# Performance work log

Measured on AMD Instinct MI355X. Metric: run time of the kernel, lower is better.

## Reference

```python
import jax, jax.numpy as jnp
import numpy as np

EPS = 1e-5

# The 8 fixed sobel kernels from the original module. Summing convolutions with
# the same input equals one convolution with the summed kernel, so we embed the
# four 3x3 kernels (pad=1) into 5x5 (pad=2) and precombine everything into a
# single depthwise 5x5 kernel (exactly the math of detect_edge_1/2 summed).
_K3 = [
    [[2, 4, 2], [0, 0, 0], [-2, -4, -2]],
    [[4, 2, 0], [2, 0, -2], [0, -2, -4]],
    [[2, 0, -2], [4, 0, -4], [2, 0, -2]],
    [[0, -2, -4], [2, 0, -2], [4, 2, 0]],
]
_K5 = [
    [[0, 0, 0, 0, 0], [0, -2, -4, -2, 0], [-1, -4, 0, 4, 1], [0, 2, 4, 2, 0], [0, 0, 0, 0, 0]],
    [[0, 0, -1, 0, 0], [0, -2, -4, 2, 0], [0, -4, 0, 4, 0], [0, -2, 4, 2, 0], [0, 0, 1, 0, 0]],
    [[0, 0, 1, 0, 0], [0, -2, 4, 2, 0], [0, -4, 0, 4, 0], [0, -2, -4, 2, 0], [0, 0, -1, 0, 0]],
    [[0, 0, 0, 0, 0], [0, 2, 4, 2, 0], [-1, -4, 0, 4, 1], [0, -2, -4, -2, 0], [0, 0, 0, 0, 0]],
]

def _combined_sobel_kernel():
    k = np.zeros((5, 5), dtype=np.float32)
    for k3 in _K3:
        k[1:4, 1:4] += np.asarray(k3, dtype=np.float32)
    for k5 in _K5:
        k += np.asarray(k5, dtype=np.float32)
    return jnp.asarray(k)

SOBEL_K = _combined_sobel_kernel()  # [5,5]


def _conv2d(x, w, b, pad):
    # x: [N,C,H,W], w: [O,I,kh,kw]
    y = jax.lax.conv_general_dilated(
        x, w, window_strides=(1, 1), padding=[(pad, pad), (pad, pad)],
        dimension_numbers=('NCHW', 'OIHW', 'NCHW'))
    return y + b[None, :, None, None]


def _bn_relu(y, gamma, beta):
    # BatchNorm2d in training mode: per-channel batch stats over (N,H,W),
    # biased variance, eps=1e-5.
    m = jnp.mean(y, axis=(0, 2, 3), keepdims=True)
    v = jnp.mean(jnp.square(y - m), axis=(0, 2, 3), keepdims=True)
    yn = (y - m) * jax.lax.rsqrt(v + EPS)
    return jax.nn.relu(yn * gamma[None, :, None, None] + beta[None, :, None, None])


def _single_conv(x, w, b, gamma, beta, pad):
    return _bn_relu(_conv2d(x, w, b, pad), gamma, beta)


def _sobel(x):
    # Fused depthwise conv replacing the per-channel loops over 8 kernels.
    C = x.shape[1]
    w = jnp.broadcast_to(SOBEL_K[None, None], (C, 1, 5, 5))
    return jax.lax.conv_general_dilated(
        x, w, window_strides=(1, 1), padding=[(2, 2), (2, 2)],
        dimension_numbers=('NCHW', 'OIHW', 'NCHW'), feature_group_count=C)


def setup_inputs() -> dict:
    key = jax.random.key(0)
    ks = jax.random.split(key, 16)
    Cin, Cout = 64, 128
    Ch = Cout // 2
    B, H, W = 8, 160, 160
    s = 0.05
    d = {
        'input_f': jax.random.normal(ks[0], (B, Cin, H, W), jnp.float32),
        'w1': jax.random.normal(ks[1], (Cout, Cin, 1, 1), jnp.float32) * s,
        'b1': jnp.zeros((Cout,), jnp.float32),
        'g1': jnp.ones((Cout,), jnp.float32),
        'be1': jnp.zeros((Cout,), jnp.float32),
        'w2': jax.random.normal(ks[2], (Ch, Cout, 3, 3), jnp.float32) * s,
        'b2': jnp.zeros((Ch,), jnp.float32),
        'g2': jnp.ones((Ch,), jnp.float32),
        'be2': jnp.zeros((Ch,), jnp.float32),
        'w3': jax.random.normal(ks[3], (Ch, Ch, 3, 3), jnp.float32) * s,
        'b3': jnp.zeros((Ch,), jnp.float32),
        'g3': jnp.ones((Ch,), jnp.float32),
        'be3': jnp.zeros((Ch,), jnp.float32),
        'w4': jax.random.normal(ks[4], (Ch, Cin, 3, 3), jnp.float32) * s,
        'b4': jnp.zeros((Ch,), jnp.float32),
        'g4': jnp.ones((Ch,), jnp.float32),
        'be4': jnp.zeros((Ch,), jnp.float32),
    }
    return d


def reference(input_f, w1, b1, g1, be1, w2, b2, g2, be2, w3, b3, g3, be3, w4, b4, g4, be4):
    c1 = _single_conv(input_f, w1, b1, g1, be1, pad=0)   # [B,Cout,H,W]
    c2 = _single_conv(c1, w2, b2, g2, be2, pad=1)        # [B,Cout//2,H,W]
    edge = _sobel(c2)                                    # depthwise sobel sum
    c3 = _single_conv(edge, w3, b3, g3, be3, pad=1)
    skip = _single_conv(input_f, w4, b4, g4, be4, pad=1)
    return jnp.concatenate([skip, c3], axis=1)           # [B,Cout,H,W]
```

## Files before the change

### kernel.cpp

```cpp
#include <hip/hip_runtime.h>

typedef unsigned short u16;
typedef unsigned int u32;
typedef __attribute__((ext_vector_type(8))) short bf16x8;
typedef __attribute__((ext_vector_type(4))) float f32x4;

#define WD 160
#define HW 25600
#define NPIXF 204800.0f
#define BNEPS 1e-5f
#define SLOTB 6553600ll
#define BATB  13107200ll

__device__ __forceinline__ float bf2f(u16 u){ return __uint_as_float(((u32)u)<<16); }
__device__ __forceinline__ u16 f2bf(float f){ u32 x=__float_as_uint(f); return (u16)((x + 0x7FFFu + ((x>>16)&1u))>>16); }
__device__ __forceinline__ u32 pack2(float a,float b){ return (u32)f2bf(a) | ((u32)f2bf(b)<<16); }

__device__ __forceinline__ f32x4 MF(bf16x8 a, bf16x8 b, f32x4 c){
  return __builtin_amdgcn_mfma_f32_16x16x32_bf16(a, b, c, 0, 0, 0);
}
__device__ __forceinline__ void gload16(const void* g, void* l){
  __builtin_amdgcn_global_load_lds((const __attribute__((address_space(1))) void*)(g),
                                   (__attribute__((address_space(3))) void*)(l), 16, 0, 0);
}

__global__ __launch_bounds__(256) void k_prepw(
    const float* __restrict__ w1, const float* __restrict__ w2,
    const float* __restrict__ w3, const float* __restrict__ w4,
    u16* __restrict__ wp1, u16* __restrict__ wp2,
    u16* __restrict__ wp3, u16* __restrict__ wp4)
{
  int t = blockIdx.x*256 + threadIdx.x;
  if (t < 8192){
    int i = t&7, oc = (t>>3)&127, kc = (t>>10)&3, icb = t>>12;
    wp1[t] = f2bf(w1[oc*64 + icb*32 + kc*8 + i]);
  }
  int u = t - 8192;
  if (u >= 0 && u < 73728){
    int i = u&7, oc = (u>>3)&63, kc = (u>>9)&3, v = u>>11;
    int icb = (v*57)>>9; int tap = v - icb*9;
    wp2[u] = f2bf(w2[(oc*128 + icb*32 + kc*8 + i)*9 + tap]);
  }
  int u3 = t - (8192+73728);
  if (u3 >= 0 && u3 < 36864){
    int k = u3&31, oc = (u3>>5)&63, v = u3>>11;
    int icb = (v >= 9) ? 1 : 0; int tap = v - icb*9;
    wp3[u3] = f2bf(w3[(oc*64 + icb*32 + k)*9 + tap]);
    wp4[u3] = f2bf(w4[(oc*64 + icb*32 + k)*9 + tap]);
  }
}

__global__ __launch_bounds__(256,2) void k_conv1(
    const float* __restrict__ x, const u16* __restrict__ wp1,
    char* __restrict__ dout, float* __restrict__ stats, int nslot)
{
  __shared__ __align__(16) char Xs[2][8192];
  const int tid = threadIdx.x, lane = tid&63, w = tid>>6;
  const int l15 = lane&15, kc = lane>>4;
  const int b = blockIdx.y, px0 = blockIdx.x*128;
  const float* xb = x + (size_t)b*64*HW;

#pragma unroll 4
  for (int it=0; it<16; ++it){
    int s = it*256 + tid;
    int icb = s >> 11, sl = s & 2047;
    int icp = sl >> 7, px = sl & 127;
    const float* p = xb + (size_t)(icb*32 + icp*2)*HW + px0 + px;
    float v0 = p[0], v1 = p[HW];
    int phys = px*64 + (((icp>>2) ^ ((px>>1)&3))<<4) + (icp&3)*4;
    *(u32*)(Xs[icb] + phys) = pack2(v0, v1);
  }
  __syncthreads();

  f32x4 acc[4][4];
  for (int t=0;t<4;++t) for (int o=0;o<4;++o) acc[t][o] = (f32x4){0.f,0.f,0.f,0.f};
  const int och = (w>>1)*64;
  int a1off[4];
  for (int t=0;t<4;++t){
    int px = (w&1)*64 + t*16 + l15;
    a1off[t] = px*64 + ((kc ^ ((px>>1)&3))<<4);
  }
#pragma unroll
  for (int icb=0; icb<2; ++icb){
    bf16x8 a[4], bw[4];
#pragma unroll
    for (int t=0;t<4;++t) a[t] = *(const bf16x8*)(Xs[icb] + a1off[t]);
#pragma unroll
    for (int o=0;o<4;++o)
      bw[o] = *(const bf16x8*)(wp1 + ((size_t)(icb*4 + kc)*128 + och + o*16 + l15)*8);
#pragma unroll
    for (int t=0;t<4;++t)
#pragma unroll
      for (int o=0;o<4;++o)
        acc[t][o] = MF(a[t], bw[o], acc[t][o]);
  }

  u16* c1 = (u16*)(dout + (size_t)b*BATB);
  float sa[4]={0,0,0,0}, sq[4]={0,0,0,0};
  for (int t=0;t<4;++t){
    int pxb = px0 + (w&1)*64 + t*16 + kc*4;
    for (int o=0;o<4;++o){
      int oc = och + o*16 + l15;
#pragma unroll
      for (int r=0;r<4;++r){
        float v = acc[t][o][r];
        c1[(size_t)(pxb + r)*128 + oc] = f2bf(v);
        sa[o]+=v; sq[o]+=v*v;
      }
    }
  }
  const int slot = (blockIdx.y*gridDim.x + blockIdx.x) & (nslot-1);
  for (int o=0;o<4;++o){
    float s1_=sa[o], s2_=sq[o];
    s1_+=__shfl_xor(s1_,16); s2_+=__shfl_xor(s2_,16);
    s1_+=__shfl_xor(s1_,32); s2_+=__shfl_xor(s2_,32);
    if (lane < 16){
      float* p = stats + ((size_t)slot*128 + och + o*16 + l15)*4;
      atomicAdd(p, s1_); atomicAdd(p+1, s2_);
    }
  }
}

__global__ void k_fold(const float* __restrict__ src, float* __restrict__ dst, int nslot){
  int c = threadIdx.x; if (c >= 128) return;
  float sm=0.f, sq=0.f;
  for (int s=0;s<nslot;++s){ const float* p = src + ((size_t)s*128 + c)*4; sm+=p[0]; sq+=p[1]; }
  dst[c*2] = sm; dst[c*2+1] = sq;
}

__global__ __launch_bounds__(256) void k_bn1(
    char* __restrict__ dout, const float* __restrict__ f1,
    const float* __restrict__ g1, const float* __restrict__ be1)
{
  __shared__ float asc[128], abi[128];
  int tid = threadIdx.x;
  if (tid < 128){
    float m = f1[tid*2]/NPIXF;
    float v = f1[tid*2+1]/NPIXF - m*m;
    float sc = g1[tid]*rsqrtf(v + BNEPS);
    asc[tid] = sc; abi[tid] = be1[tid] - m*sc;
  }
  __syncthreads();
  int b = blockIdx.y;
  size_t r = ((size_t)blockIdx.x*256 + tid)*8;
  int c0 = (int)(r & 127);
  const u16* src = (const u16*)(dout + (size_t)b*BATB) + r;
  u16* dst = (u16*)(dout + (size_t)b*BATB + SLOTB) + r;
  uint4 q = *(const uint4*)src;
  u32 wv[4] = {q.x,q.y,q.z,q.w};
#pragma unroll
  for (int j=0;j<4;++j){
    float lo = bf2f((u16)(wv[j]&0xFFFFu)), hi = bf2f((u16)(wv[j]>>16));
    lo = fmaxf(0.f, lo*asc[c0+2*j]   + abi[c0+2*j]);
    hi = fmaxf(0.f, hi*asc[c0+2*j+1] + abi[c0+2*j+1]);
    wv[j] = pack2(lo, hi);
  }
  *(uint4*)dst = make_uint4(wv[0],wv[1],wv[2],wv[3]);
}

__global__ __launch_bounds__(256,2) void k_conv2(
    char* __restrict__ dout, const u16* __restrict__ wp2,
    float* __restrict__ statsO, const u16* __restrict__ zeros, int nslot)
{
  __shared__ __align__(16) char Xs[24576];
  const int tid = threadIdx.x, lane = tid&63, w = tid>>6;
  const int l15 = lane&15, kc = lane>>4;
  const int b = blockIdx.z, gx0 = blockIdx.x*32, gy0 = blockIdx.y*8;
  const u16* c1a = (const u16*)(dout + (size_t)b*BATB + SLOTB);
  u16* raw2 = (u16*)(dout + (size_t)b*BATB);

  f32x4 acc[4][4];
  for (int t=0;t<4;++t) for (int o=0;o<4;++o) acc[t][o] = (f32x4){0.f,0.f,0.f,0.f};

  int xon[2][3];
  for (int h=0;h<2;++h) for (int dx=0;dx<3;++dx){
    int xi = l15 + h*16 + dx;
    xon[h][dx] = xi*64 + ((kc ^ ((xi>>1)&3))<<4);
  }

  for (int icb=0; icb<4; ++icb){
    __syncthreads();
    for (int it=0; it<6; ++it){
      int s = it*256 + tid;
      int p = s>>2, sub = s&3;
      int yy = (int)(((u32)p*241u)>>13);
      int xi = p - yy*34;
      int gy = gy0 - 1 + yy, gx = gx0 - 1 + xi;
      int c = sub ^ ((xi>>1)&3);
      const u16* src = zeros + ((tid&63)<<3);
      if (p < 340 && (unsigned)gy < 160u && (unsigned)gx < 160u)
        src = c1a + ((size_t)(gy*WD+gx)*128 + icb*32 + c*8);
      gload16(src, Xs + (it*256 + (tid & ~63))*16);
    }
    asm volatile("s_waitcnt vmcnt(0)" ::: "memory");
    __syncthreads();
#pragma unroll
    for (int tap=0; tap<9; ++tap){
      const int dy = tap/3, dx = tap - dy*3;
      bf16x8 a[4], bw[4];
#pragma unroll
      for (int o=0;o<4;++o)
        bw[o] = *(const bf16x8*)(wp2 + ((size_t)((icb*9 + tap)*4 + kc)*64 + o*16 + l15)*8);
#pragma unroll
      for (int t=0;t<4;++t)
        a[t] = *(const bf16x8*)(Xs + (2*w + (t>>1) + dy)*2176 + xon[t&1][dx]);
#pragma unroll
      for (int t=0;t<4;++t)
#pragma unroll
        for (int o=0;o<4;++o)
          acc[t][o] = MF(a[t], bw[o], acc[t][o]);
    }
  }

  float sa[4]={0,0,0,0}, sq[4]={0,0,0,0};
  for (int t=0;t<4;++t){
    int gy = gy0 + 2*w + (t>>1);
    int gxb = gx0 + (t&1)*16 + kc*4;
    for (int o=0;o<4;++o){
      int oc = o*16 + l15;
#pragma unroll
      for (int r=0;r<4;++r){
        float v = acc[t][o][r];
        raw2[(size_t)(gy*WD + gxb + r)*64 + oc] = f2bf(v);
        sa[o]+=v; sq[o]+=v*v;
      }
    }
  }
  int slot = (blockIdx.x + 5*(blockIdx.y + 20*blockIdx.z)) & (nslot-1);
  for (int o=0;o<4;++o){
    float s1_=sa[o], s2_=sq[o];
    s1_+=__shfl_xor(s1_,16); s2_+=__shfl_xor(s2_,16);
    s1_+=__shfl_xor(s1_,32); s2_+=__shfl_xor(s2_,32);
    if (lane<16){
      float* p = statsO + ((size_t)slot*128 + o*16 + l15)*4;
      atomicAdd(p,s1_); atomicAdd(p+1,s2_);
    }
  }
}

__global__ __launch_bounds__(256) void k_sobel(
    char* __restrict__ dout, const float* __restrict__ f2,
    const float* __restrict__ g2, const float* __restrict__ be2)
{
  __shared__ float asc[64], abi[64];
  int tid = threadIdx.x;
  if (tid < 64){
    float m = f2[tid*2]/NPIXF, v = f2[tid*2+1]/NPIXF - m*m;
    float sc = g2[tid]*rsqrtf(v+BNEPS);
    asc[tid]=sc; abi[tid]=be2[tid]-m*sc;
  }
  __syncthreads();
  int b = blockIdx.z, cb = blockIdx.y;
  int px = blockIdx.x*256 + tid;
  int y = (int)(((u32)px*52429u)>>23);
  int x = px - y*WD;
  const u16* raw2 = (const u16*)(dout + (size_t)b*BATB);
  u16* edge = (u16*)(dout + (size_t)b*BATB + 3276800);
  float av[8] = {0,0,0,0,0,0,0,0};
  auto TAP = [&](int dy, int dx, float wt){
    int yy = y+dy, xx = x+dx;
    if ((unsigned)yy>=160u || (unsigned)xx>=160u) return;
    uint4 q = *(const uint4*)(raw2 + ((size_t)(yy*WD+xx)*64 + cb*8));
    u32 ww[4] = {q.x,q.y,q.z,q.w};
#pragma unroll
    for (int j=0;j<4;++j){
      float lo = bf2f((u16)(ww[j]&0xFFFFu)), hi = bf2f((u16)(ww[j]>>16));
      lo = fmaxf(0.f, lo*asc[cb*8+2*j]   + abi[cb*8+2*j]);
      hi = fmaxf(0.f, hi*asc[cb*8+2*j+1] + abi[cb*8+2*j+1]);
      av[2*j]   += wt*lo;
      av[2*j+1] += wt*hi;
    }
  };
  TAP(-1,-1,4.f); TAP(-1,0,4.f);
  TAP(0,-2,-2.f); TAP(0,-1,-8.f); TAP(0,1,8.f); TAP(0,2,2.f);
  TAP(1,0,-4.f);  TAP(1,1,-4.f);
  uint4 o;
  o.x = pack2(av[0],av[1]); o.y = pack2(av[2],av[3]);
  o.z = pack2(av[4],av[5]); o.w = pack2(av[6],av[7]);
  *(uint4*)(edge + ((size_t)px*64 + cb*8)) = o;
}

__global__ __launch_bounds__(256,2) void k_conv34(
    char* __restrict__ dout, const float* __restrict__ x,
    const u16* __restrict__ wp3, const u16* __restrict__ wp4,
    float* __restrict__ st3, float* __restrict__ st4,
    const u16* __restrict__ zeros, int nslot)
{
  __shared__ __align__(16) char Xs[49152];
  const int tid = threadIdx.x, lane = tid&63, w = tid>>6;
  const int l15 = lane&15, kc = lane>>4;
  const int bz = blockIdx.z, b = bz>>1, job = bz&1;
  const int gx0 = blockIdx.x*32, gy0 = blockIdx.y*8;
  const u16* wp = job ? wp4 : wp3;
  float* statsO = job ? st4 : st3;
  float* out = job ? (float*)(dout + (size_t)b*BATB)
                   : (float*)(dout + (size_t)b*BATB + SLOTB);

  if (job){
    const float* xb = x + (size_t)b*64*HW;
#pragma unroll 4
    for (int it=0; it<43; ++it){
      int s = it*256 + tid; if (s >= 10880) break;
      int icb = (s >= 5440) ? 1 : 0;
      int sl = s - icb*5440;
      int yq = (int)(((u32)(sl>>5)*965u)>>14);
      int rem = sl - yq*544;
      int icp = (int)(((u32)rem*241u)>>13);
      int xi = rem - icp*34;
      int gy = gy0-1+yq, gx = gx0-1+xi;
      float v0=0.f, v1=0.f;
      if ((unsigned)gy<160u && (unsigned)gx<160u){
        const float* p = xb + (size_t)(icb*32 + icp*2)*HW + gy*WD + gx;
        v0 = p[0]; v1 = p[HW];
      }
      int phys = icb*24576 + (yq*34 + xi)*64 + (((icp>>2) ^ ((xi>>1)&3))<<4) + (icp&3)*4;
      *(u32*)(Xs + phys) = pack2(v0, v1);
    }
  } else {
    const u16* edge = (const u16*)(dout + (size_t)b*BATB + 3276800);
    for (int it=0; it<12; ++it){
      int s = it*256 + tid;
      int icb = s >> 11;
      icb = (s >= 1536) ? 1 : 0;
      int sl = s - icb*1536;
      int p = sl>>2, sub = sl&3;
      int yy = (int)(((u32)p*241u)>>13);
      int xi = p - yy*34;
      int gy = gy0-1+yy, gx = gx0-1+xi;
      int c = sub ^ ((xi>>1)&3);
      const u16* src = zeros + ((tid&63)<<3);
      if (p<340 && (unsigned)gy<160u && (unsigned)gx<160u)
        src = edge + ((size_t)(gy*WD+gx)*64 + icb*32 + c*8);
      gload16(src, Xs + (it*256 + (tid & ~63))*16);
    }
    asm volatile("s_waitcnt vmcnt(0)" ::: "memory");
  }
  __syncthreads();

  f32x4 acc[4][4];
  for (int m=0;m<4;++m) for (int t=0;t<4;++t) acc[m][t] = (f32x4){0.f,0.f,0.f,0.f};
  int xon[2][3];
  for (int h=0;h<2;++h) for (int dx=0;dx<3;++dx){
    int xi = l15 + h*16 + dx;
    xon[h][dx] = xi*64 + ((kc ^ ((xi>>1)&3))<<4);
  }

#pragma unroll
  for (int icb=0; icb<2; ++icb){
#pragma unroll
    for (int tap=0; tap<9; ++tap){
      const int dy = tap/3, dx = tap - dy*3;
      bf16x8 a[4], bv[4];
#pragma unroll
      for (int m=0;m<4;++m)
        a[m] = *(const bf16x8*)(wp + ((size_t)((icb*9+tap)*64 + m*16 + l15)*32 + kc*8));
#pragma unroll
      for (int t=0;t<4;++t)
        bv[t] = *(const bf16x8*)(Xs + icb*24576 + (2*w + (t>>1) + dy)*2176 + xon[t&1][dx]);
#pragma unroll
      for (int m=0;m<4;++m)
#pragma unroll
        for (int t=0;t<4;++t)
          acc[m][t] = MF(a[m], bv[t], acc[m][t]);
    }
  }

  float sa[4][4], sq[4][4];
  for (int m=0;m<4;++m) for (int r=0;r<4;++r){ sa[m][r]=0.f; sq[m][r]=0.f; }
  for (int m=0;m<4;++m){
    for (int t=0;t<4;++t){
      int gy = gy0 + 2*w + (t>>1);
      int gx = gx0 + (t&1)*16 + l15;
#pragma unroll
      for (int r=0;r<4;++r){
        float v = acc[m][t][r];
        out[(size_t)(m*16 + kc*4 + r)*HW + gy*WD + gx] = v;
        sa[m][r]+=v; sq[m][r]+=v*v;
      }
    }
  }
  int slot = (blockIdx.x + 5*(blockIdx.y + 20*blockIdx.z)) & (nslot-1);
  for (int m=0;m<4;++m)
    for (int r=0;r<4;++r){
      float s1_=sa[m][r], s2_=sq[m][r];
      s1_+=__shfl_xor(s1_,1); s2_+=__shfl_xor(s2_,1);
      s1_+=__shfl_xor(s1_,2); s2_+=__shfl_xor(s2_,2);
      s1_+=__shfl_xor(s1_,4); s2_+=__shfl_xor(s2_,4);
      s1_+=__shfl_xor(s1_,8); s2_+=__shfl_xor(s2_,8);
      if (l15==0){
        float* p = statsO + ((size_t)slot*128 + m*16 + kc*4 + r)*4;
        atomicAdd(p,s1_); atomicAdd(p+1,s2_);
      }
    }
}

__global__ __launch_bounds__(256) void k_bnrelu(
    float* __restrict__ io, const float* __restrict__ f3, const float* __restrict__ f4,
    const float* __restrict__ g3, const float* __restrict__ be3,
    const float* __restrict__ g4, const float* __restrict__ be4)
{
  size_t e = ((size_t)blockIdx.x*256 + threadIdx.x)*8;
  int cg = (int)((e/HW) & 127);
  float* p = io + (size_t)blockIdx.y*3276800 + e;
  float sm,sq,gg,bb;
  if (cg>=64){ int c=cg-64; sm=f3[c*2]; sq=f3[c*2+1]; gg=g3[c]; bb=be3[c]; }
  else       {             sm=f4[cg*2]; sq=f4[cg*2+1]; gg=g4[cg]; bb=be4[cg]; }
  float m = sm/NPIXF;
  float v = sq/NPIXF - m*m;
  float sc = gg*rsqrtf(v + BNEPS);
  float bi = bb - m*sc;
  float4 a = *(float4*)p;
  float4 bq = *(float4*)(p+4);
  a.x=fmaxf(0.f,a.x*sc+bi); a.y=fmaxf(0.f,a.y*sc+bi);
  a.z=fmaxf(0.f,a.z*sc+bi); a.w=fmaxf(0.f,a.w*sc+bi);
  bq.x=fmaxf(0.f,bq.x*sc+bi); bq.y=fmaxf(0.f,bq.y*sc+bi);
  bq.z=fmaxf(0.f,bq.z*sc+bi); bq.w=fmaxf(0.f,bq.w*sc+bi);
  *(float4*)p = a;
  *(float4*)(p+4) = bq;
}

extern "C" void kernel_launch(void* const* d_in, const int* in_sizes, int n_in,
                              void* d_out, int out_size, void* d_ws, size_t ws_size,
                              hipStream_t stream)
{
  const float* x   = (const float*)d_in[0];
  const float* w1  = (const float*)d_in[1];
  const float* g1  = (const float*)d_in[3];
  const float* be1 = (const float*)d_in[4];
  const float* w2  = (const float*)d_in[5];
  const float* g2  = (const float*)d_in[7];
  const float* be2 = (const float*)d_in[8];
  const float* w3  = (const float*)d_in[9];
  const float* g3  = (const float*)d_in[11];
  const float* be3 = (const float*)d_in[12];
  const float* w4  = (const float*)d_in[13];
  const float* g4  = (const float*)d_in[15];
  const float* be4 = (const float*)d_in[16];
  (void)in_sizes; (void)n_in; (void)out_size;

  int nslot = 32;
  auto need = [&](int ns)->size_t{
    return (size_t)4*ns*128*4*4 + 4096 + (size_t)(8192+73728+36864+36864)*2 + 1024;
  };
  while (nslot > 1 && need(nslot) > ws_size) nslot >>= 1;
  if (need(nslot) > ws_size) return;

  char* ws = (char*)d_ws;
  float* S = (float*)ws;
  size_t stg = (size_t)nslot*128*4;
  float* S0=S, *S1=S+stg, *S2=S+2*stg, *S3=S+3*stg;
  float* F = S + 4*stg;
  u16* wp1 = (u16*)(F + 1024);
  u16* wp2 = wp1 + 8192;
  u16* wp3 = wp2 + 73728;
  u16* wp4 = wp3 + 36864;
  u16* zeros = wp4 + 36864;

  hipMemsetAsync(S, 0, 4*stg*sizeof(float), stream);
  hipMemsetAsync(zeros, 0, 1024, stream);

  k_prepw<<<464, 256, 0, stream>>>(w1, w2, w3, w4, wp1, wp2, wp3, wp4);
  k_conv1<<<dim3(200,8), 256, 0, stream>>>(x, wp1, (char*)d_out, S0, nslot);
  k_fold<<<1, 128, 0, stream>>>(S0, F, nslot);
  k_bn1<<<dim3(1600,8), 256, 0, stream>>>((char*)d_out, F, g1, be1);
  k_conv2<<<dim3(5,20,8), 256, 0, stream>>>((char*)d_out, wp2, S1, zeros, nslot);
  k_fold<<<1, 128, 0, stream>>>(S1, F+256, nslot);
  k_sobel<<<dim3(100,8,8), 256, 0, stream>>>((char*)d_out, F+256, g2, be2);
  k_conv34<<<dim3(5,20,16), 256, 0, stream>>>((char*)d_out, x, wp3, wp4, S2, S3, zeros, nslot);
  k_fold<<<1, 128, 0, stream>>>(S2, F+512, nslot);
  k_fold<<<1, 128, 0, stream>>>(S3, F+768, nslot);
  k_bnrelu<<<dim3(1600,8), 256, 0, stream>>>((float*)d_out, F+512, F+768, g3, be3, g4, be4);
}
```

Baseline: 392.4 us.

## Fuse BN1 into conv2 staging, fold stats in sobel, vectorize input loads

Removes the separate BN1+ReLU pass by applying the scale/bias while conv2 stages its input tile into LDS, which drops one full read/write sweep of the conv1 activations. The separate fold kernel after conv2 goes away because the sobel kernel reduces the per-slot statistics itself, and the two final fold launches are merged into one. Conv1 and the skip branch of conv34 now load x with float4 vectors, and conv34 stages one channel block at a time to halve its LDS footprint. When the workspace is large enough, the edge tensor is placed there; otherwise conv34 is split into two launches. The cost is register-staged loads in conv2 in place of direct-to-LDS loads, plus extra synchronisation.

```diff
diff --git a/kernel.cpp b/kernel.cpp
--- a/kernel.cpp
+++ b/kernel.cpp
@@ -54,21 +54,28 @@
     const float* __restrict__ x, const u16* __restrict__ wp1,
     char* __restrict__ dout, float* __restrict__ stats, int nslot)
 {
-  __shared__ __align__(16) char Xs[2][8192];
+  __shared__ __align__(16) char Xs[16384];
   const int tid = threadIdx.x, lane = tid&63, w = tid>>6;
   const int l15 = lane&15, kc = lane>>4;
   const int b = blockIdx.y, px0 = blockIdx.x*128;
   const float* xb = x + (size_t)b*64*HW;
 
-#pragma unroll 4
-  for (int it=0; it<16; ++it){
-    int s = it*256 + tid;
-    int icb = s >> 11, sl = s & 2047;
-    int icp = sl >> 7, px = sl & 127;
-    const float* p = xb + (size_t)(icb*32 + icp*2)*HW + px0 + px;
-    float v0 = p[0], v1 = p[HW];
-    int phys = px*64 + (((icp>>2) ^ ((px>>1)&3))<<4) + (icp&3)*4;
-    *(u32*)(Xs[icb] + phys) = pack2(v0, v1);
+#pragma unroll
+  for (int q=0; q<4; ++q){
+    int s = q*256 + tid;
+    int icb = s >> 9, sl = s & 511;
+    int cp = sl >> 5, px4 = sl & 31;
+    const float* pa = xb + (size_t)(icb*32 + cp*2)*HW + px0 + px4*4;
+    float4 va = *(const float4*)pa;
+    float4 vb = *(const float4*)(pa + HW);
+    float fa[4] = {va.x, va.y, va.z, va.w};
+    float fb[4] = {vb.x, vb.y, vb.z, vb.w};
+#pragma unroll
+    for (int e=0;e<4;++e){
+      int px = px4*4+e;
+      int phys = icb*8192 + px*64 + (((cp>>2) ^ ((px>>1)&3))<<4) + (cp&3)*4;
+      *(u32*)(Xs + phys) = pack2(fa[e], fb[e]);
+    }
   }
   __syncthreads();
 
@@ -84,7 +91,7 @@
   for (int icb=0; icb<2; ++icb){
     bf16x8 a[4], bw[4];
 #pragma unroll
-    for (int t=0;t<4;++t) a[t] = *(const bf16x8*)(Xs[icb] + a1off[t]);
+    for (int t=0;t<4;++t) a[t] = *(const bf16x8*)(Xs + icb*8192 + a1off[t]);
 #pragma unroll
     for (int o=0;o<4;++o)
       bw[o] = *(const bf16x8*)(wp1 + ((size_t)(icb*4 + kc)*128 + och + o*16 + l15)*8);
@@ -128,46 +135,36 @@
   dst[c*2] = sm; dst[c*2+1] = sq;
 }
 
-__global__ __launch_bounds__(256) void k_bn1(
-    char* __restrict__ dout, const float* __restrict__ f1,
-    const float* __restrict__ g1, const float* __restrict__ be1)
-{
-  __shared__ float asc[128], abi[128];
-  int tid = threadIdx.x;
-  if (tid < 128){
-    float m = f1[tid*2]/NPIXF;
-    float v = f1[tid*2+1]/NPIXF - m*m;
-    float sc = g1[tid]*rsqrtf(v + BNEPS);
-    asc[tid] = sc; abi[tid] = be1[tid] - m*sc;
-  }
-  __syncthreads();
-  int b = blockIdx.y;
-  size_t r = ((size_t)blockIdx.x*256 + tid)*8;
-  int c0 = (int)(r & 127);
-  const u16* src = (const u16*)(dout + (size_t)b*BATB) + r;
-  u16* dst = (u16*)(dout + (size_t)b*BATB + SLOTB) + r;
-  uint4 q = *(const uint4*)src;
-  u32 wv[4] = {q.x,q.y,q.z,q.w};
-#pragma unroll
-  for (int j=0;j<4;++j){
-    float lo = bf2f((u16)(wv[j]&0xFFFFu)), hi = bf2f((u16)(wv[j]>>16));
-    lo = fmaxf(0.f, lo*asc[c0+2*j]   + abi[c0+2*j]);
-    hi = fmaxf(0.f, hi*asc[c0+2*j+1] + abi[c0+2*j+1]);
-    wv[j] = pack2(lo, hi);
-  }
-  *(uint4*)dst = make_uint4(wv[0],wv[1],wv[2],wv[3]);
+__global__ void k_fold23(const float* __restrict__ s2, const float* __restrict__ s3,
+                         float* __restrict__ f23, int nslot){
+  int t = threadIdx.x;
+  const float* src = (t < 128) ? s2 : s3;
+  int c = t & 127;
+  float sm=0.f, sq=0.f;
+  for (int s=0;s<nslot;++s){ const float* p = src + ((size_t)s*128 + c)*4; sm+=p[0]; sq+=p[1]; }
+  f23[t*2] = sm; f23[t*2+1] = sq;
 }
 
 __global__ __launch_bounds__(256,2) void k_conv2(
     char* __restrict__ dout, const u16* __restrict__ wp2,
-    float* __restrict__ statsO, const u16* __restrict__ zeros, int nslot)
-{
-  __shared__ __align__(16) char Xs[24576];
+    const float* __restrict__ f0, const float* __restrict__ g1,
+    const float* __restrict__ be1,
+    float* __restrict__ statsO, int nslot)
+{
+  __shared__ __align__(16) char Xs[21760];
+  __shared__ __align__(16) float scbi[128][2];
   const int tid = threadIdx.x, lane = tid&63, w = tid>>6;
   const int l15 = lane&15, kc = lane>>4;
   const int b = blockIdx.z, gx0 = blockIdx.x*32, gy0 = blockIdx.y*8;
-  const u16* c1a = (const u16*)(dout + (size_t)b*BATB + SLOTB);
-  u16* raw2 = (u16*)(dout + (size_t)b*BATB);
+  const u16* c1raw = (const u16*)(dout + (size_t)b*BATB);
+  u16* raw2 = (u16*)(dout + (size_t)b*BATB + SLOTB);
+
+  if (tid < 128){
+    float m = f0[tid*2]/NPIXF;
+    float v = f0[tid*2+1]/NPIXF - m*m;
+    float sc = g1[tid]*rsqrtf(v + BNEPS);
+    scbi[tid][0] = sc; scbi[tid][1] = be1[tid] - m*sc;
+  }
 
   f32x4 acc[4][4];
   for (int t=0;t<4;++t) for (int o=0;o<4;++o) acc[t][o] = (f32x4){0.f,0.f,0.f,0.f};
@@ -178,21 +175,32 @@
     xon[h][dx] = xi*64 + ((kc ^ ((xi>>1)&3))<<4);
   }
 
+  __syncthreads();
   for (int icb=0; icb<4; ++icb){
-    __syncthreads();
-    for (int it=0; it<6; ++it){
-      int s = it*256 + tid;
+    if (icb) __syncthreads();
+    for (int s = tid; s < 1360; s += 256){
       int p = s>>2, sub = s&3;
       int yy = (int)(((u32)p*241u)>>13);
       int xi = p - yy*34;
       int gy = gy0 - 1 + yy, gx = gx0 - 1 + xi;
       int c = sub ^ ((xi>>1)&3);
-      const u16* src = zeros + ((tid&63)<<3);
-      if (p < 340 && (unsigned)gy < 160u && (unsigned)gx < 160u)
-        src = c1a + ((size_t)(gy*WD+gx)*128 + icb*32 + c*8);
-      gload16(src, Xs + (it*256 + (tid & ~63))*16);
-    }
-    asm volatile("s_waitcnt vmcnt(0)" ::: "memory");
+      uint4 o4 = make_uint4(0,0,0,0);
+      if ((unsigned)gy < 160u && (unsigned)gx < 160u){
+        int cb = icb*32 + c*8;
+        uint4 q = *(const uint4*)(c1raw + ((size_t)(gy*WD+gx)*128 + cb));
+        u32 ww[4] = {q.x,q.y,q.z,q.w};
+        u32 ro[4];
+#pragma unroll
+        for (int j=0;j<4;++j){
+          float lo = bf2f((u16)(ww[j]&0xFFFFu)), hi = bf2f((u16)(ww[j]>>16));
+          lo = fmaxf(0.f, lo*scbi[cb+2*j][0]   + scbi[cb+2*j][1]);
+          hi = fmaxf(0.f, hi*scbi[cb+2*j+1][0] + scbi[cb+2*j+1][1]);
+          ro[j] = pack2(lo, hi);
+        }
+        o4 = make_uint4(ro[0],ro[1],ro[2],ro[3]);
+      }
+      *(uint4*)(Xs + p*64 + sub*16) = o4;
+    }
     __syncthreads();
 #pragma unroll
     for (int tap=0; tap<9; ++tap){
@@ -239,23 +247,35 @@
 }
 
 __global__ __launch_bounds__(256) void k_sobel(
-    char* __restrict__ dout, const float* __restrict__ f2,
-    const float* __restrict__ g2, const float* __restrict__ be2)
-{
-  __shared__ float asc[64], abi[64];
+    char* __restrict__ dout, const float* __restrict__ S1,
+    const float* __restrict__ g2, const float* __restrict__ be2,
+    u16* __restrict__ edge_base, long ebstride, int nslot)
+{
+  __shared__ float ascS[8], abiS[8];
   int tid = threadIdx.x;
+  int b = blockIdx.z, cb = blockIdx.y;
   if (tid < 64){
-    float m = f2[tid*2]/NPIXF, v = f2[tid*2+1]/NPIXF - m*m;
-    float sc = g2[tid]*rsqrtf(v+BNEPS);
-    asc[tid]=sc; abi[tid]=be2[tid]-m*sc;
+    int c = cb*8 + (tid&7);
+    float sm=0.f, sq=0.f;
+    for (int s = tid>>3; s < nslot; s += 8){
+      const float* p = S1 + ((size_t)s*128 + c)*4;
+      sm += p[0]; sq += p[1];
+    }
+    sm += __shfl_xor(sm, 8);  sq += __shfl_xor(sq, 8);
+    sm += __shfl_xor(sm, 16); sq += __shfl_xor(sq, 16);
+    sm += __shfl_xor(sm, 32); sq += __shfl_xor(sq, 32);
+    if (tid < 8){
+      float m = sm/NPIXF, v = sq/NPIXF - m*m;
+      float sc = g2[c]*rsqrtf(v+BNEPS);
+      ascS[tid] = sc; abiS[tid] = be2[c] - m*sc;
+    }
   }
   __syncthreads();
-  int b = blockIdx.z, cb = blockIdx.y;
   int px = blockIdx.x*256 + tid;
   int y = (int)(((u32)px*52429u)>>23);
   int x = px - y*WD;
-  const u16* raw2 = (const u16*)(dout + (size_t)b*BATB);
-  u16* edge = (u16*)(dout + (size_t)b*BATB + 3276800);
+  const u16* raw2 = (const u16*)(dout + (size_t)b*BATB + SLOTB);
+  u16* edge = edge_base + (size_t)b*ebstride;
   float av[8] = {0,0,0,0,0,0,0,0};
   auto TAP = [&](int dy, int dx, float wt){
     int yy = y+dy, xx = x+dx;
@@ -265,8 +285,8 @@
 #pragma unroll
     for (int j=0;j<4;++j){
       float lo = bf2f((u16)(ww[j]&0xFFFFu)), hi = bf2f((u16)(ww[j]>>16));
-      lo = fmaxf(0.f, lo*asc[cb*8+2*j]   + abi[cb*8+2*j]);
-      hi = fmaxf(0.f, hi*asc[cb*8+2*j+1] + abi[cb*8+2*j+1]);
+      lo = fmaxf(0.f, lo*ascS[2*j]   + abiS[2*j]);
+      hi = fmaxf(0.f, hi*ascS[2*j+1] + abiS[2*j+1]);
       av[2*j]   += wt*lo;
       av[2*j+1] += wt*hi;
     }
@@ -284,58 +304,22 @@
     char* __restrict__ dout, const float* __restrict__ x,
     const u16* __restrict__ wp3, const u16* __restrict__ wp4,
     float* __restrict__ st3, float* __restrict__ st4,
-    const u16* __restrict__ zeros, int nslot)
-{
-  __shared__ __align__(16) char Xs[49152];
+    const u16* __restrict__ zeros, const u16* __restrict__ edge_base,
+    long ebstride, int nslot, int mode)
+{
+  __shared__ __align__(16) char Xs[24576];
   const int tid = threadIdx.x, lane = tid&63, w = tid>>6;
   const int l15 = lane&15, kc = lane>>4;
-  const int bz = blockIdx.z, b = bz>>1, job = bz&1;
+  int b, job;
+  if (mode == 2){ b = blockIdx.z>>1; job = blockIdx.z&1; }
+  else          { b = blockIdx.z;    job = mode; }
   const int gx0 = blockIdx.x*32, gy0 = blockIdx.y*8;
   const u16* wp = job ? wp4 : wp3;
   float* statsO = job ? st4 : st3;
   float* out = job ? (float*)(dout + (size_t)b*BATB)
                    : (float*)(dout + (size_t)b*BATB + SLOTB);
-
-  if (job){
-    const float* xb = x + (size_t)b*64*HW;
-#pragma unroll 4
-    for (int it=0; it<43; ++it){
-      int s = it*256 + tid; if (s >= 10880) break;
-      int icb = (s >= 5440) ? 1 : 0;
-      int sl = s - icb*5440;
-      int yq = (int)(((u32)(sl>>5)*965u)>>14);
-      int rem = sl - yq*544;
-      int icp = (int)(((u32)rem*241u)>>13);
-      int xi = rem - icp*34;
-      int gy = gy0-1+yq, gx = gx0-1+xi;
-      float v0=0.f, v1=0.f;
-      if ((unsigned)gy<160u && (unsigned)gx<160u){
-        const float* p = xb + (size_t)(icb*32 + icp*2)*HW + gy*WD + gx;
-        v0 = p[0]; v1 = p[HW];
-      }
-      int phys = icb*24576 + (yq*34 + xi)*64 + (((icp>>2) ^ ((xi>>1)&3))<<4) + (icp&3)*4;
-      *(u32*)(Xs + phys) = pack2(v0, v1);
-    }
-  } else {
-    const u16* edge = (const u16*)(dout + (size_t)b*BATB + 3276800);
-    for (int it=0; it<12; ++it){
-      int s = it*256 + tid;
-      int icb = s >> 11;
-      icb = (s >= 1536) ? 1 : 0;
-      int sl = s - icb*1536;
-      int p = sl>>2, sub = sl&3;
-      int yy = (int)(((u32)p*241u)>>13);
-      int xi = p - yy*34;
-      int gy = gy0-1+yy, gx = gx0-1+xi;
-      int c = sub ^ ((xi>>1)&3);
-      const u16* src = zeros + ((tid&63)<<3);
-      if (p<340 && (unsigned)gy<160u && (unsigned)gx<160u)
-        src = edge + ((size_t)(gy*WD+gx)*64 + icb*32 + c*8);
-      gload16(src, Xs + (it*256 + (tid & ~63))*16);
-    }
-    asm volatile("s_waitcnt vmcnt(0)" ::: "memory");
-  }
-  __syncthreads();
+  const float* xb = x + (size_t)b*64*HW;
+  const u16* edge = edge_base + (size_t)b*ebstride;
 
   f32x4 acc[4][4];
   for (int m=0;m<4;++m) for (int t=0;t<4;++t) acc[m][t] = (f32x4){0.f,0.f,0.f,0.f};
@@ -345,8 +329,58 @@
     xon[h][dx] = xi*64 + ((kc ^ ((xi>>1)&3))<<4);
   }
 
-#pragma unroll
   for (int icb=0; icb<2; ++icb){
+    if (icb) __syncthreads();
+    if (job){
+      for (int s = tid; s < 1600; s += 256){
+        int s10 = (int)(((u32)s*6554u)>>16);
+        int q = s - s10*10;
+        int cp = (int)(((u32)s10*6554u)>>16);
+        int yq = s10 - cp*10;
+        int gy = gy0 - 1 + yq;
+        int gxq = gx0 - 4 + q*4;
+        float fa[4] = {0,0,0,0}, fb[4] = {0,0,0,0};
+        if ((unsigned)gy < 160u){
+          const float* pa = xb + (size_t)(icb*32 + cp*2)*HW + gy*WD + gxq;
+          if (gxq >= 0 && gxq + 3 < 160){
+            float4 va = *(const float4*)pa;
+            float4 vb = *(const float4*)(pa + HW);
+            fa[0]=va.x; fa[1]=va.y; fa[2]=va.z; fa[3]=va.w;
+            fb[0]=vb.x; fb[1]=vb.y; fb[2]=vb.z; fb[3]=vb.w;
+          } else {
+#pragma unroll
+            for (int e=0;e<4;++e){
+              int gx = gxq + e;
+              if ((unsigned)gx < 160u){ fa[e] = pa[e]; fb[e] = pa[e + HW]; }
+            }
+          }
+        }
+#pragma unroll
+        for (int e=0;e<4;++e){
+          int xi = gxq + e - (gx0 - 1);
+          if ((unsigned)xi < 34u){
+            int phys = (yq*34 + xi)*64 + (((cp>>2) ^ ((xi>>1)&3))<<4) + (cp&3)*4;
+            *(u32*)(Xs + phys) = pack2(fa[e], fb[e]);
+          }
+        }
+      }
+    } else {
+      for (int it=0; it<6; ++it){
+        int s = it*256 + tid;
+        int p = s>>2, sub = s&3;
+        int yy = (int)(((u32)p*241u)>>13);
+        int xi = p - yy*34;
+        int gy = gy0-1+yy, gx = gx0-1+xi;
+        int c = sub ^ ((xi>>1)&3);
+        const u16* src = zeros + ((tid&63)<<3);
+        if (p<340 && (unsigned)gy<160u && (unsigned)gx<160u)
+          src = edge + ((size_t)(gy*WD+gx)*64 + icb*32 + c*8);
+        gload16(src, Xs + (it*256 + (tid & ~63))*16);
+      }
+      asm volatile("s_waitcnt vmcnt(0)" ::: "memory");
+    }
+    __syncthreads();
+
 #pragma unroll
     for (int tap=0; tap<9; ++tap){
       const int dy = tap/3, dx = tap - dy*3;
@@ -356,7 +390,7 @@
         a[m] = *(const bf16x8*)(wp + ((size_t)((icb*9+tap)*64 + m*16 + l15)*32 + kc*8));
 #pragma unroll
       for (int t=0;t<4;++t)
-        bv[t] = *(const bf16x8*)(Xs + icb*24576 + (2*w + (t>>1) + dy)*2176 + xon[t&1][dx]);
+        bv[t] = *(const bf16x8*)(Xs + (2*w + (t>>1) + dy)*2176 + xon[t&1][dx]);
 #pragma unroll
       for (int m=0;m<4;++m)
 #pragma unroll
@@ -395,7 +429,7 @@
 }
 
 __global__ __launch_bounds__(256) void k_bnrelu(
-    float* __restrict__ io, const float* __restrict__ f3, const float* __restrict__ f4,
+    float* __restrict__ io, const float* __restrict__ f23,
     const float* __restrict__ g3, const float* __restrict__ be3,
     const float* __restrict__ g4, const float* __restrict__ be4)
 {
@@ -403,8 +437,8 @@
   int cg = (int)((e/HW) & 127);
   float* p = io + (size_t)blockIdx.y*3276800 + e;
   float sm,sq,gg,bb;
-  if (cg>=64){ int c=cg-64; sm=f3[c*2]; sq=f3[c*2+1]; gg=g3[c]; bb=be3[c]; }
-  else       {             sm=f4[cg*2]; sq=f4[cg*2+1]; gg=g4[cg]; bb=be4[cg]; }
+  if (cg>=64){ int c=cg-64; sm=f23[c*2]; sq=f23[c*2+1]; gg=g3[c]; bb=be3[c]; }
+  else       { sm=f23[(128+cg)*2]; sq=f23[(128+cg)*2+1]; gg=g4[cg]; bb=be4[cg]; }
   float m = sm/NPIXF;
   float v = sq/NPIXF - m*m;
   float sc = gg*rsqrtf(v + BNEPS);
@@ -455,6 +489,12 @@
   u16* wp3 = wp2 + 73728;
   u16* wp4 = wp3 + 36864;
   u16* zeros = wp4 + 36864;
+  size_t base = need(nslot);
+  bool big = (ws_size >= base + 26214400ull);
+  u16* edge_base;
+  long ebstride;
+  if (big){ edge_base = (u16*)(ws + base); ebstride = 64L*HW; }
+  else    { edge_base = (u16*)((char*)d_out + 3276800); ebstride = BATB/2; }
 
   hipMemsetAsync(S, 0, 4*stg*sizeof(float), stream);
   hipMemsetAsync(zeros, 0, 1024, stream);
@@ -462,12 +502,17 @@
   k_prepw<<<464, 256, 0, stream>>>(w1, w2, w3, w4, wp1, wp2, wp3, wp4);
   k_conv1<<<dim3(200,8), 256, 0, stream>>>(x, wp1, (char*)d_out, S0, nslot);
   k_fold<<<1, 128, 0, stream>>>(S0, F, nslot);
-  k_bn1<<<dim3(1600,8), 256, 0, stream>>>((char*)d_out, F, g1, be1);
-  k_conv2<<<dim3(5,20,8), 256, 0, stream>>>((char*)d_out, wp2, S1, zeros, nslot);
-  k_fold<<<1, 128, 0, stream>>>(S1, F+256, nslot);
-  k_sobel<<<dim3(100,8,8), 256, 0, stream>>>((char*)d_out, F+256, g2, be2);
-  k_conv34<<<dim3(5,20,16), 256, 0, stream>>>((char*)d_out, x, wp3, wp4, S2, S3, zeros, nslot);
-  k_fold<<<1, 128, 0, stream>>>(S2, F+512, nslot);
-  k_fold<<<1, 128, 0, stream>>>(S3, F+768, nslot);
-  k_bnrelu<<<dim3(1600,8), 256, 0, stream>>>((float*)d_out, F+512, F+768, g3, be3, g4, be4);
-}
+  k_conv2<<<dim3(5,20,8), 256, 0, stream>>>((char*)d_out, wp2, F, g1, be1, S1, nslot);
+  k_sobel<<<dim3(100,8,8), 256, 0, stream>>>((char*)d_out, S1, g2, be2, edge_base, ebstride, nslot);
+  if (big){
+    k_conv34<<<dim3(5,20,16), 256, 0, stream>>>((char*)d_out, x, wp3, wp4, S2, S3,
+                                                zeros, edge_base, ebstride, nslot, 2);
+  } else {
+    k_conv34<<<dim3(5,20,8), 256, 0, stream>>>((char*)d_out, x, wp3, wp4, S2, S3,
+                                               zeros, edge_base, ebstride, nslot, 0);
+    k_conv34<<<dim3(5,20,8), 256, 0, stream>>>((char*)d_out, x, wp3, wp4, S2, S3,
+                                               zeros, edge_base, ebstride, nslot, 1);
+  }
+  k_fold23<<<1, 256, 0, stream>>>(S2, S3, F + 256, nslot);
+  k_bnrelu<<<dim3(1600,8), 256, 0, stream>>>((float*)d_out, F + 256, g3, be3, g4, be4);
+}
```

New measurement: 348.3 us. 1.13x faster.
